# Kernel tuning notes

Hardware: AMD Instinct MI355X
Metric: run time of the kernel (lower is better)

## Reference

```python
import jax, jax.numpy as jnp
import numpy as np

N_HEADS = 8

def _rotate_half(x):
    # interleaved pairs: (x1, x2) -> (-x2, x1), rotary_embedding_torch style
    x = x.reshape(*x.shape[:-1], -1, 2)
    x1, x2 = x[..., 0], x[..., 1]
    return jnp.stack([-x2, x1], axis=-1).reshape(*x.shape[:-2], -1)

def _apply_rotary(freqs, t):
    # freqs: (seq, d), t: (..., seq, d)
    return t * jnp.cos(freqs) + _rotate_half(t) * jnp.sin(freqs)

def _sdpa(q, k, v):
    # q,k,v: (b, g, h, s, d) ; attention over s
    d = q.shape[-1]
    scores = jnp.einsum('bghqd,bghkd->bghqk', q, k) / jnp.sqrt(jnp.asarray(d, q.dtype))
    w = jax.nn.softmax(scores, axis=-1)
    return jnp.einsum('bghqk,bghkd->bghqd', w, v)

def setup_inputs() -> dict:
    key = jax.random.key(0)
    ks = jax.random.split(key, 5)
    B, T, Fd, D = 4, 256, 64, 256
    x = jax.random.normal(ks[0], (B, T, Fd, D), dtype=jnp.float32)
    W_attn = jax.random.normal(ks[1], (D, 5 * D), dtype=jnp.float32) * 0.02
    W_proj = jax.random.normal(ks[2], (D, D), dtype=jnp.float32) * 0.02
    hd = D // N_HEADS
    rotary_t = jax.random.uniform(ks[3], (T, hd), dtype=jnp.float32) * 2 * np.pi
    rotary_f = jax.random.uniform(ks[4], (Fd, hd), dtype=jnp.float32) * 2 * np.pi
    return {"x": x, "W_attn": W_attn, "W_proj": W_proj,
            "rotary_t": rotary_t, "rotary_f": rotary_f}

def reference(x, W_attn, W_proj, rotary_t, rotary_f):
    B, T, Fd, D = x.shape
    h = N_HEADS
    d = D // h
    # fused QKV: (B,T,F,5D) -> (5, B, h, T, F, d)
    qkv = (x @ W_attn).reshape(B, T, Fd, 5, h, d).transpose(3, 0, 4, 1, 2, 5)
    q_t, q_f, k_t, k_f, v = qkv[0], qkv[1], qkv[2], qkv[3], qkv[4]
    # ---- time attention: batch over (b, f), attend over t ----
    # b h t f d -> b f h t d
    q_t = jnp.transpose(q_t, (0, 3, 1, 2, 4))
    k_t = jnp.transpose(k_t, (0, 3, 1, 2, 4))
    v_t = jnp.transpose(v, (0, 3, 1, 2, 4))
    q_t = _apply_rotary(rotary_t, q_t)
    k_t = _apply_rotary(rotary_t, k_t)
    v_t = _sdpa(q_t, k_t, v_t)  # (b, f, h, t, d)
    # ---- frequency attention: batch over (b, t), attend over f ----
    # b h t f d -> b t h f d
    q_f = jnp.transpose(q_f, (0, 2, 1, 3, 4))
    k_f = jnp.transpose(k_f, (0, 2, 1, 3, 4))
    # b f h t d -> b t h f d
    v_f = jnp.transpose(v_t, (0, 3, 2, 1, 4))
    q_f = _apply_rotary(rotary_f, q_f)
    k_f = _apply_rotary(rotary_f, k_f)
    y = _sdpa(q_f, k_f, v_f)  # (b, t, h, f, d)
    # b t h f d -> b t f (h d)
    y = jnp.transpose(y, (0, 1, 3, 2, 4)).reshape(B, T, Fd, D)
    return y @ W_proj
```

## Files before the change

### kernel.cpp

```cpp
#include <hip/hip_runtime.h>

typedef unsigned short u16;
typedef unsigned int u32;
typedef short s16x8 __attribute__((ext_vector_type(8)));
typedef u16 u16x4 __attribute__((ext_vector_type(4)));
typedef float f32x4 __attribute__((ext_vector_type(4)));
typedef u32 u32x2 __attribute__((ext_vector_type(2)));
typedef u32 u32x4 __attribute__((ext_vector_type(4)));

#define MFMA(a,b,c) __builtin_amdgcn_mfma_f32_16x16x32_bf16((a),(b),(c),0,0,0)

static const size_t PL = 16777216;

__device__ __forceinline__ float b2f(u16 b) {
    return __uint_as_float(((unsigned int)b) << 16);
}
__device__ __forceinline__ u16 f2b(float f) {
    unsigned int u = __float_as_uint(f);
    unsigned int r = (u + 0x7FFFu + ((u >> 16) & 1u)) >> 16;
    return (u16)r;
}
__device__ __forceinline__ u32 cvtpk(float lo, float hi) {
    u32 r;
    asm("v_cvt_pk_bf16_f32 %0, %1, %2" : "=v"(r) : "v"(lo), "v"(hi));
    return r;
}
__device__ __forceinline__ float fexp2(float x) {
#if __has_builtin(__builtin_amdgcn_exp2f)
    return __builtin_amdgcn_exp2f(x);
#else
    return exp2f(x);
#endif
}

__device__ __forceinline__ s16x8 rot8(const u16* __restrict__ src,
                                      const float* __restrict__ cp,
                                      const float* __restrict__ sp) {
    s16x8 u = *(const s16x8*)src;
    f32x4 c0 = *(const f32x4*)cp, c1 = *(const f32x4*)(cp + 4);
    f32x4 s0 = *(const f32x4*)sp, s1 = *(const f32x4*)(sp + 4);
    float x[8];
#pragma unroll
    for (int j = 0; j < 8; j++) x[j] = b2f((u16)u[j]);
    float c[8] = {c0[0], c0[1], c0[2], c0[3], c1[0], c1[1], c1[2], c1[3]};
    float s[8] = {s0[0], s0[1], s0[2], s0[3], s1[0], s1[1], s1[2], s1[3]};
    u32x4 r;
#pragma unroll
    for (int p = 0; p < 4; p++) {
        float e = x[2 * p], o = x[2 * p + 1];
        float lo = e * c[2 * p] - o * s[2 * p];
        float hi = fmaf(e, s[2 * p + 1], o * c[2 * p + 1]);
        r[p] = cvtpk(lo, hi);
    }
    return __builtin_bit_cast(s16x8, r);
}

__global__ void prep_x_k(const float* __restrict__ x, u16* __restrict__ xb) {
    size_t i = ((size_t)blockIdx.x * 256 + threadIdx.x) * 8;
    f32x4 a = *(const f32x4*)(x + i);
    f32x4 b = *(const f32x4*)(x + i + 4);
    u32x4 o = { cvtpk(a[0], a[1]), cvtpk(a[2], a[3]), cvtpk(b[0], b[1]), cvtpk(b[2], b[3]) };
    *(u32x4*)(xb + i) = o;
}

__global__ void prep_aux_k(const float* __restrict__ Wa, const float* __restrict__ Wp,
                           const float* __restrict__ rt, const float* __restrict__ rf,
                           u16* __restrict__ wt_a, u16* __restrict__ wt_p,
                           float* __restrict__ ct_t, float* __restrict__ st_t,
                           float* __restrict__ ct_f, float* __restrict__ st_f) {
    int i = blockIdx.x * 256 + threadIdx.x;
    if (i < 81920) {
        int idx = i * 4;
        int k = idx / 1280, n = idx - k * 1280;
        f32x4 v = *(const f32x4*)&Wa[idx];
#pragma unroll
        for (int j = 0; j < 4; j++) wt_a[(n + j) * 256 + k] = f2b(v[j]);
    } else if (i < 98304) {
        int idx = (i - 81920) * 4;
        int k = idx >> 8, n = idx & 255;
        f32x4 v = *(const f32x4*)&Wp[idx];
#pragma unroll
        for (int j = 0; j < 4; j++) wt_p[(n + j) * 256 + k] = f2b(v[j]);
    } else if (i < 100352) {
        int j = (i - 98304) * 4;
        f32x4 v = *(const f32x4*)&rt[j];
        f32x4 c, s;
#pragma unroll
        for (int jj = 0; jj < 4; jj++) { float ss, cc; __sincosf(v[jj], &ss, &cc); c[jj] = cc; s[jj] = ss; }
        *(f32x4*)&ct_t[j] = c; *(f32x4*)&st_t[j] = s;
    } else if (i < 100864) {
        int j = (i - 100352) * 4;
        f32x4 v = *(const f32x4*)&rf[j];
        f32x4 c, s;
#pragma unroll
        for (int jj = 0; jj < 4; jj++) { float ss, cc; __sincosf(v[jj], &ss, &cc); c[jj] = cc; s[jj] = ss; }
        *(f32x4*)&ct_f[j] = c; *(f32x4*)&st_f[j] = s;
    }
}

template<int NT, bool TO_PLANES>
__global__ __launch_bounds__(256, 2) void gemm_k(const u16* __restrict__ A,
                                                 const u16* __restrict__ Bt,
                                                 u16* __restrict__ outp,
                                                 float* __restrict__ outf) {
    __shared__ __align__(16) u16 As[2][128][72];
    __shared__ __align__(16) u16 Bs[2][128][72];
    int bid = blockIdx.x;
    int xcd = bid & 7, slot = bid >> 3;
    int L = xcd * ((512 * NT) / 8) + slot;
    int mt = L / NT, nt = L - mt * NT;
    int m0 = mt * 128, n0 = nt * 128;
    int tid = threadIdx.x, lane = tid & 63, w = tid >> 6;
    int wm = w >> 1, wn = w & 1;
    int g = lane >> 4, lr = lane & 15;
    f32x4 acc[4][4] = {};
    s16x8 apb[4], bpb[4];

    auto loadAB = [&](int k0) {
#pragma unroll
        for (int i = 0; i < 4; i++) {
            int c = tid + i * 256, row = c >> 3, p = (c & 7) * 8;
            apb[i] = *(const s16x8*)&A[(size_t)(m0 + row) * 256 + k0 + p];
            bpb[i] = *(const s16x8*)&Bt[(size_t)(n0 + row) * 256 + k0 + p];
        }
    };
    auto storeAB = [&](int buf) {
#pragma unroll
        for (int i = 0; i < 4; i++) {
            int c = tid + i * 256, row = c >> 3, p = (c & 7) * 8;
            *(s16x8*)&As[buf][row][p] = apb[i];
            *(s16x8*)&Bs[buf][row][p] = bpb[i];
        }
    };

    loadAB(0);
    storeAB(0);
    loadAB(64);
    __syncthreads();

    for (int s = 0; s < 4; s++) {
        int cur = s & 1;
        s16x8 af0[4], bf0[4];
#pragma unroll
        for (int mi = 0; mi < 4; mi++) af0[mi] = *(const s16x8*)&As[cur][wm * 64 + mi * 16 + lr][g * 8];
#pragma unroll
        for (int ni = 0; ni < 4; ni++) bf0[ni] = *(const s16x8*)&Bs[cur][wn * 64 + ni * 16 + lr][g * 8];
        if (s < 3) storeAB(cur ^ 1);
        if (s < 2) loadAB((s + 2) * 64);
#pragma unroll
        for (int ni = 0; ni < 4; ni++)
#pragma unroll
            for (int mi = 0; mi < 4; mi++)
                acc[ni][mi] = MFMA(bf0[ni], af0[mi], acc[ni][mi]);
        s16x8 af1[4], bf1[4];
#pragma unroll
        for (int mi = 0; mi < 4; mi++) af1[mi] = *(const s16x8*)&As[cur][wm * 64 + mi * 16 + lr][32 + g * 8];
#pragma unroll
        for (int ni = 0; ni < 4; ni++) bf1[ni] = *(const s16x8*)&Bs[cur][wn * 64 + ni * 16 + lr][32 + g * 8];
#pragma unroll
        for (int ni = 0; ni < 4; ni++)
#pragma unroll
            for (int mi = 0; mi < 4; mi++)
                acc[ni][mi] = MFMA(bf1[ni], af1[mi], acc[ni][mi]);
        __syncthreads();
    }

#pragma unroll
    for (int ni = 0; ni < 4; ni++) {
#pragma unroll
        for (int mi = 0; mi < 4; mi++) {
            int token = m0 + wm * 64 + mi * 16 + lr;
            int n = n0 + wn * 64 + ni * 16 + g * 4;
            if (TO_PLANES) {
                u32x2 pk = { cvtpk(acc[ni][mi][0], acc[ni][mi][1]),
                             cvtpk(acc[ni][mi][2], acc[ni][mi][3]) };
                int pl = n >> 8, c = n & 255, h = c >> 5, d0 = c & 31;
                int b = token >> 14, t = (token >> 6) & 255, f = token & 63;
                size_t addr = (pl == 1 || pl == 3)
                    ? ((size_t)(((b * 256 + t) * 8 + h) * 64 + f) * 32 + d0)
                    : ((size_t)(((b * 64 + f) * 8 + h) * 256 + t) * 32 + d0);
                *(u32x2*)&outp[(size_t)pl * PL + addr] = pk;
            } else {
                *(f32x4*)&outf[(size_t)token * 256 + n] = acc[ni][mi];
            }
        }
    }
}

__global__ __launch_bounds__(256, 3) void attn_time_k(const u16* __restrict__ qt,
                                                      const u16* __restrict__ kt,
                                                      const u16* __restrict__ vp,
                                                      u16* __restrict__ y1,
                                                      const float* __restrict__ ct,
                                                      const float* __restrict__ st) {
    __shared__ __align__(16) u16 K_l[256][40];
    __shared__ __align__(16) u16 Vt[32][264];
    __shared__ __align__(16) u16 Pst[4][2][16][40];
    int bid = blockIdx.x;
    int xcd = bid & 7, slot = bid >> 3;
    int L = xcd * 512 + slot;
    int qh = L & 1, head = L >> 1;
    int h = head & 7, f = (head >> 3) & 63, b = head >> 9;
    int tid = threadIdx.x, lane = tid & 63, w = tid >> 6;
    int g = lane >> 4, lr = lane & 15;
    const u16* Khead = kt + (size_t)head * 8192;
    const u16* Qhead = qt + (size_t)head * 8192;
    const u16* Vhead = vp + (size_t)head * 8192;

#pragma unroll
    for (int i = 0; i < 4; i++) {
        int c = tid + i * 256;
        int t = c >> 2, p = (c & 3) * 8;
        *(s16x8*)&K_l[t][p] = rot8(Khead + t * 32 + p, ct + t * 32 + p, st + t * 32 + p);
    }
    {
        int ka = (tid & 63) * 4, db = (tid >> 6) * 8;
        const u16* vb = Vhead + (size_t)ka * 32 + db;
        s16x8 r0 = *(const s16x8*)(vb);
        s16x8 r1 = *(const s16x8*)(vb + 32);
        s16x8 r2 = *(const s16x8*)(vb + 64);
        s16x8 r3 = *(const s16x8*)(vb + 96);
#pragma unroll
        for (int dd = 0; dd < 8; dd++) {
            u16x4 pk = { (u16)r0[dd], (u16)r1[dd], (u16)r2[dd], (u16)r3[dd] };
            *(u16x4*)&Vt[db + dd][ka] = pk;
        }
    }
    int qbase = qh * 128 + w * 32;
    s16x8 qf_[2];
#pragma unroll
    for (int qi = 0; qi < 2; qi++) {
        int q = qbase + qi * 16 + lr;
        qf_[qi] = rot8(Qhead + q * 32 + g * 8, ct + q * 32 + g * 8, st + q * 32 + g * 8);
    }
    __syncthreads();

    f32x4 sT[16][2] = {};
#pragma unroll
    for (int ki = 0; ki < 16; ki++) {
        s16x8 kf8 = *(const s16x8*)&K_l[ki * 16 + lr][g * 8];
        sT[ki][0] = MFMA(kf8, qf_[0], sT[ki][0]);
        sT[ki][1] = MFMA(kf8, qf_[1], sT[ki][1]);
    }
    const float sc2 = 0.17677669529663687f * 1.4426950408889634f;
    float rsum[2];
#pragma unroll
    for (int qi = 0; qi < 2; qi++) {
        float m = -1e30f;
#pragma unroll
        for (int ki = 0; ki < 16; ki++)
#pragma unroll
            for (int r = 0; r < 4; r++) m = fmaxf(m, sT[ki][qi][r]);
        m = fmaxf(m, __shfl_xor(m, 16));
        m = fmaxf(m, __shfl_xor(m, 32));
        float msc = m * sc2;
        float ssum = 0.f;
#pragma unroll
        for (int ki = 0; ki < 16; ki++)
#pragma unroll
            for (int r = 0; r < 4; r++) {
                float p = fexp2(sT[ki][qi][r] * sc2 - msc);
                sT[ki][qi][r] = p; ssum += p;
            }
        ssum += __shfl_xor(ssum, 16);
        ssum += __shfl_xor(ssum, 32);
        rsum[qi] = 1.0f / ssum;
    }

    f32x4 o_[2][2] = {};
#pragma unroll
    for (int ks = 0; ks < 8; ks++) {
        s16x8 vf0 = *(const s16x8*)&Vt[lr][ks * 32 + g * 8];
        s16x8 vf1 = *(const s16x8*)&Vt[16 + lr][ks * 32 + g * 8];
#pragma unroll
        for (int qi = 0; qi < 2; qi++) {
            u32x2 w0 = { cvtpk(sT[2 * ks][qi][0], sT[2 * ks][qi][1]),
                         cvtpk(sT[2 * ks][qi][2], sT[2 * ks][qi][3]) };
            u32x2 w1 = { cvtpk(sT[2 * ks + 1][qi][0], sT[2 * ks + 1][qi][1]),
                         cvtpk(sT[2 * ks + 1][qi][2], sT[2 * ks + 1][qi][3]) };
            *(u32x2*)&Pst[w][qi][lr][g * 4] = w0;
            *(u32x2*)&Pst[w][qi][lr][16 + g * 4] = w1;
            s16x8 pf = *(const s16x8*)&Pst[w][qi][lr][g * 8];
            o_[0][qi] = MFMA(vf0, pf, o_[0][qi]);
            o_[1][qi] = MFMA(vf1, pf, o_[1][qi]);
        }
    }
#pragma unroll
    for (int qi = 0; qi < 2; qi++) {
        int q = qbase + qi * 16 + lr;
        float rs = rsum[qi];
        u16* dst = y1 + ((size_t)(((b * 256 + q) * 8 + h) * 64 + f)) * 32;
#pragma unroll
        for (int di = 0; di < 2; di++) {
            u32x2 ob = { cvtpk(o_[di][qi][0] * rs, o_[di][qi][1] * rs),
                         cvtpk(o_[di][qi][2] * rs, o_[di][qi][3] * rs) };
            *(u32x2*)&dst[di * 16 + g * 4] = ob;
        }
    }
}

__global__ __launch_bounds__(256, 2) void attn_freq_k(const u16* __restrict__ qfp,
                                                      const u16* __restrict__ kfp,
                                                      const u16* __restrict__ y1,
                                                      u16* __restrict__ y2,
                                                      const float* __restrict__ ct,
                                                      const float* __restrict__ st) {
    __shared__ __align__(16) u16 K_l[4][64][40];
    __shared__ __align__(16) u16 Vt[4][32][72];
    __shared__ __align__(16) u16 Pst[4][2][16][40];
    int tid = threadIdx.x, lane = tid & 63, w = tid >> 6;
    int g = lane >> 4, lr = lane & 15;
    int head = blockIdx.x * 4 + w;
    int h = head & 7, t = (head >> 3) & 255, b = head >> 11;
    const u16* Khead = kfp + (size_t)head * 2048;
    const u16* Qhead = qfp + (size_t)head * 2048;
    const u16* Vhead = y1 + (size_t)head * 2048;

#pragma unroll
    for (int i = 0; i < 4; i++) {
        int c = i * 64 + lane;
        int row = c >> 2, p = (c & 3) * 8;
        *(s16x8*)&K_l[w][row][p] = rot8(Khead + row * 32 + p, ct + row * 32 + p, st + row * 32 + p);
    }
    {
        int ka = lr * 4, db = g * 8;
        const u16* vb = Vhead + (size_t)ka * 32 + db;
        s16x8 r0 = *(const s16x8*)(vb);
        s16x8 r1 = *(const s16x8*)(vb + 32);
        s16x8 r2 = *(const s16x8*)(vb + 64);
        s16x8 r3 = *(const s16x8*)(vb + 96);
#pragma unroll
        for (int dd = 0; dd < 8; dd++) {
            u16x4 pk = { (u16)r0[dd], (u16)r1[dd], (u16)r2[dd], (u16)r3[dd] };
            *(u16x4*)&Vt[w][db + dd][ka] = pk;
        }
    }
    s16x8 qfr[4];
#pragma unroll
    for (int qi = 0; qi < 4; qi++) {
        int q = qi * 16 + lr;
        qfr[qi] = rot8(Qhead + q * 32 + g * 8, ct + q * 32 + g * 8, st + q * 32 + g * 8);
    }

    f32x4 sT[4][4] = {};
#pragma unroll
    for (int ki = 0; ki < 4; ki++) {
        s16x8 kf8 = *(const s16x8*)&K_l[w][ki * 16 + lr][g * 8];
#pragma unroll
        for (int qi = 0; qi < 4; qi++) sT[ki][qi] = MFMA(kf8, qfr[qi], sT[ki][qi]);
    }
    const float sc2 = 0.17677669529663687f * 1.4426950408889634f;
    float rsum[4];
#pragma unroll
    for (int qi = 0; qi < 4; qi++) {
        float m = -1e30f;
#pragma unroll
        for (int ki = 0; ki < 4; ki++)
#pragma unroll
            for (int r = 0; r < 4; r++) m = fmaxf(m, sT[ki][qi][r]);
        m = fmaxf(m, __shfl_xor(m, 16));
        m = fmaxf(m, __shfl_xor(m, 32));
        float msc = m * sc2;
        float ssum = 0.f;
#pragma unroll
        for (int ki = 0; ki < 4; ki++)
#pragma unroll
            for (int r = 0; r < 4; r++) {
                float p = fexp2(sT[ki][qi][r] * sc2 - msc);
                sT[ki][qi][r] = p; ssum += p;
            }
        ssum += __shfl_xor(ssum, 16);
        ssum += __shfl_xor(ssum, 32);
        rsum[qi] = 1.0f / ssum;
    }

    f32x4 o_[2][4] = {};
#pragma unroll
    for (int ks = 0; ks < 2; ks++) {
        s16x8 vf0 = *(const s16x8*)&Vt[w][lr][ks * 32 + g * 8];
        s16x8 vf1 = *(const s16x8*)&Vt[w][16 + lr][ks * 32 + g * 8];
#pragma unroll
        for (int qi = 0; qi < 4; qi++) {
            u32x2 w0 = { cvtpk(sT[2 * ks][qi][0], sT[2 * ks][qi][1]),
                         cvtpk(sT[2 * ks][qi][2], sT[2 * ks][qi][3]) };
            u32x2 w1 = { cvtpk(sT[2 * ks + 1][qi][0], sT[2 * ks + 1][qi][1]),
                         cvtpk(sT[2 * ks + 1][qi][2], sT[2 * ks + 1][qi][3]) };
            *(u32x2*)&Pst[w][qi & 1][lr][g * 4] = w0;
            *(u32x2*)&Pst[w][qi & 1][lr][16 + g * 4] = w1;
            s16x8 pf = *(const s16x8*)&Pst[w][qi & 1][lr][g * 8];
            o_[0][qi] = MFMA(vf0, pf, o_[0][qi]);
            o_[1][qi] = MFMA(vf1, pf, o_[1][qi]);
        }
    }
#pragma unroll
    for (int qi = 0; qi < 4; qi++) {
        int q = qi * 16 + lr;
        float rs = rsum[qi];
        u16* dst = y2 + ((size_t)((b * 256 + t) * 64 + q)) * 256 + h * 32;
#pragma unroll
        for (int di = 0; di < 2; di++) {
            u32x2 ob = { cvtpk(o_[di][qi][0] * rs, o_[di][qi][1] * rs),
                         cvtpk(o_[di][qi][2] * rs, o_[di][qi][3] * rs) };
            *(u32x2*)&dst[di * 16 + g * 4] = ob;
        }
    }
}

extern "C" void kernel_launch(void* const* d_in, const int* in_sizes, int n_in,
                              void* d_out, int out_size, void* d_ws, size_t ws_size,
                              hipStream_t stream) {
    const float* x  = (const float*)d_in[0];
    const float* Wa = (const float*)d_in[1];
    const float* Wp = (const float*)d_in[2];
    const float* rt = (const float*)d_in[3];
    const float* rf = (const float*)d_in[4];
    float* out = (float*)d_out;

    u16* planes = (u16*)d_ws;
    u16* qt  = planes;
    u16* qfp = planes + PL;
    u16* ktp = planes + 2 * PL;
    u16* kfp = planes + 3 * PL;
    u16* vp  = planes + 4 * PL;
    u16* y1  = planes + 5 * PL;
    u16* xb  = y1;
    u16* y2  = ktp;
    float* ct_t = (float*)(planes + 6 * PL);
    float* st_t = ct_t + 8192;
    float* ct_f = st_t + 8192;
    float* st_f = ct_f + 2048;
    u16* wt_a = (u16*)(st_f + 2048);
    u16* wt_p = wt_a + 327680;

    prep_x_k<<<8192, 256, 0, stream>>>(x, xb);
    prep_aux_k<<<394, 256, 0, stream>>>(Wa, Wp, rt, rf, wt_a, wt_p, ct_t, st_t, ct_f, st_f);
    gemm_k<10, true><<<5120, 256, 0, stream>>>(xb, wt_a, planes, nullptr);
    attn_time_k<<<4096, 256, 0, stream>>>(qt, ktp, vp, y1, ct_t, st_t);
    attn_freq_k<<<2048, 256, 0, stream>>>(qfp, kfp, y1, y2, ct_f, st_f);
    gemm_k<2, false><<<1024, 256, 0, stream>>>(y2, wt_p, nullptr, out);
}
```

Measured before the change: 211.5 us.

## Fuse fp32-to-bf16 conversion of x into QKV GEMM and merge time-attention query halves

The standalone prep_x_k pass is removed, and the QKV GEMM now loads fp32 x directly, converting to bf16 before staging into shared memory. This drops a full write and re-read of the 32 MB-scale bf16 copy of x, at the cost of twice the global load traffic per A tile inside the GEMM and more registers. Separately, attn_time_k now processes both query halves for a head in one block, halving the grid. This avoids rebuilding the rotated K and transposed V tiles twice per head but reduces parallelism and serialises the two halves.

```diff
diff --git a/kernel.cpp b/kernel.cpp
--- a/kernel.cpp
+++ b/kernel.cpp
@@ -53,14 +53,6 @@
         r[p] = cvtpk(lo, hi);
     }
     return __builtin_bit_cast(s16x8, r);
-}
-
-__global__ void prep_x_k(const float* __restrict__ x, u16* __restrict__ xb) {
-    size_t i = ((size_t)blockIdx.x * 256 + threadIdx.x) * 8;
-    f32x4 a = *(const f32x4*)(x + i);
-    f32x4 b = *(const f32x4*)(x + i + 4);
-    u32x4 o = { cvtpk(a[0], a[1]), cvtpk(a[2], a[3]), cvtpk(b[0], b[1]), cvtpk(b[2], b[3]) };
-    *(u32x4*)(xb + i) = o;
 }
 
 __global__ void prep_aux_k(const float* __restrict__ Wa, const float* __restrict__ Wp,
@@ -98,13 +90,15 @@
     }
 }
 
-template<int NT, bool TO_PLANES>
-__global__ __launch_bounds__(256, 2) void gemm_k(const u16* __restrict__ A,
+template<int NT, bool AF32, bool TO_PLANES>
+__global__ __launch_bounds__(256, 2) void gemm_k(const void* __restrict__ Ap,
                                                  const u16* __restrict__ Bt,
                                                  u16* __restrict__ outp,
                                                  float* __restrict__ outf) {
     __shared__ __align__(16) u16 As[2][128][72];
     __shared__ __align__(16) u16 Bs[2][128][72];
+    const float* Af = (const float*)Ap;
+    const u16* Ab = (const u16*)Ap;
     int bid = blockIdx.x;
     int xcd = bid & 7, slot = bid >> 3;
     int L = xcd * ((512 * NT) / 8) + slot;
@@ -114,21 +108,46 @@
     int wm = w >> 1, wn = w & 1;
     int g = lane >> 4, lr = lane & 15;
     f32x4 acc[4][4] = {};
-    s16x8 apb[4], bpb[4];
+    f32x4 apf[8]; s16x8 apb[4]; s16x8 bpb[4];
 
     auto loadAB = [&](int k0) {
+        if (AF32) {
+#pragma unroll
+            for (int i = 0; i < 8; i++) {
+                int c = tid + i * 256, row = c >> 4, cp = (c & 15) * 4;
+                apf[i] = *(const f32x4*)&Af[(size_t)(m0 + row) * 256 + k0 + cp];
+            }
+        } else {
+#pragma unroll
+            for (int i = 0; i < 4; i++) {
+                int c = tid + i * 256, row = c >> 3, p = (c & 7) * 8;
+                apb[i] = *(const s16x8*)&Ab[(size_t)(m0 + row) * 256 + k0 + p];
+            }
+        }
 #pragma unroll
         for (int i = 0; i < 4; i++) {
             int c = tid + i * 256, row = c >> 3, p = (c & 7) * 8;
-            apb[i] = *(const s16x8*)&A[(size_t)(m0 + row) * 256 + k0 + p];
             bpb[i] = *(const s16x8*)&Bt[(size_t)(n0 + row) * 256 + k0 + p];
         }
     };
     auto storeAB = [&](int buf) {
+        if (AF32) {
+#pragma unroll
+            for (int i = 0; i < 8; i++) {
+                int c = tid + i * 256, row = c >> 4, cp = (c & 15) * 4;
+                u32x2 pk = { cvtpk(apf[i][0], apf[i][1]), cvtpk(apf[i][2], apf[i][3]) };
+                *(u32x2*)&As[buf][row][cp] = pk;
+            }
+        } else {
+#pragma unroll
+            for (int i = 0; i < 4; i++) {
+                int c = tid + i * 256, row = c >> 3, p = (c & 7) * 8;
+                *(s16x8*)&As[buf][row][p] = apb[i];
+            }
+        }
 #pragma unroll
         for (int i = 0; i < 4; i++) {
             int c = tid + i * 256, row = c >> 3, p = (c & 7) * 8;
-            *(s16x8*)&As[buf][row][p] = apb[i];
             *(s16x8*)&Bs[buf][row][p] = bpb[i];
         }
     };
@@ -198,8 +217,7 @@
     __shared__ __align__(16) u16 Pst[4][2][16][40];
     int bid = blockIdx.x;
     int xcd = bid & 7, slot = bid >> 3;
-    int L = xcd * 512 + slot;
-    int qh = L & 1, head = L >> 1;
+    int head = xcd * 256 + slot;
     int h = head & 7, f = (head >> 3) & 63, b = head >> 9;
     int tid = threadIdx.x, lane = tid & 63, w = tid >> 6;
     int g = lane >> 4, lr = lane & 15;
@@ -226,75 +244,78 @@
             *(u16x4*)&Vt[db + dd][ka] = pk;
         }
     }
-    int qbase = qh * 128 + w * 32;
-    s16x8 qf_[2];
-#pragma unroll
-    for (int qi = 0; qi < 2; qi++) {
-        int q = qbase + qi * 16 + lr;
-        qf_[qi] = rot8(Qhead + q * 32 + g * 8, ct + q * 32 + g * 8, st + q * 32 + g * 8);
-    }
     __syncthreads();
 
-    f32x4 sT[16][2] = {};
-#pragma unroll
-    for (int ki = 0; ki < 16; ki++) {
-        s16x8 kf8 = *(const s16x8*)&K_l[ki * 16 + lr][g * 8];
-        sT[ki][0] = MFMA(kf8, qf_[0], sT[ki][0]);
-        sT[ki][1] = MFMA(kf8, qf_[1], sT[ki][1]);
-    }
     const float sc2 = 0.17677669529663687f * 1.4426950408889634f;
-    float rsum[2];
-#pragma unroll
-    for (int qi = 0; qi < 2; qi++) {
-        float m = -1e30f;
-#pragma unroll
-        for (int ki = 0; ki < 16; ki++)
-#pragma unroll
-            for (int r = 0; r < 4; r++) m = fmaxf(m, sT[ki][qi][r]);
-        m = fmaxf(m, __shfl_xor(m, 16));
-        m = fmaxf(m, __shfl_xor(m, 32));
-        float msc = m * sc2;
-        float ssum = 0.f;
-#pragma unroll
-        for (int ki = 0; ki < 16; ki++)
-#pragma unroll
-            for (int r = 0; r < 4; r++) {
-                float p = fexp2(sT[ki][qi][r] * sc2 - msc);
-                sT[ki][qi][r] = p; ssum += p;
-            }
-        ssum += __shfl_xor(ssum, 16);
-        ssum += __shfl_xor(ssum, 32);
-        rsum[qi] = 1.0f / ssum;
-    }
-
-    f32x4 o_[2][2] = {};
-#pragma unroll
-    for (int ks = 0; ks < 8; ks++) {
-        s16x8 vf0 = *(const s16x8*)&Vt[lr][ks * 32 + g * 8];
-        s16x8 vf1 = *(const s16x8*)&Vt[16 + lr][ks * 32 + g * 8];
+    for (int qh = 0; qh < 2; qh++) {
+        int qbase = qh * 128 + w * 32;
+        s16x8 qf_[2];
 #pragma unroll
         for (int qi = 0; qi < 2; qi++) {
-            u32x2 w0 = { cvtpk(sT[2 * ks][qi][0], sT[2 * ks][qi][1]),
-                         cvtpk(sT[2 * ks][qi][2], sT[2 * ks][qi][3]) };
-            u32x2 w1 = { cvtpk(sT[2 * ks + 1][qi][0], sT[2 * ks + 1][qi][1]),
-                         cvtpk(sT[2 * ks + 1][qi][2], sT[2 * ks + 1][qi][3]) };
-            *(u32x2*)&Pst[w][qi][lr][g * 4] = w0;
-            *(u32x2*)&Pst[w][qi][lr][16 + g * 4] = w1;
-            s16x8 pf = *(const s16x8*)&Pst[w][qi][lr][g * 8];
-            o_[0][qi] = MFMA(vf0, pf, o_[0][qi]);
-            o_[1][qi] = MFMA(vf1, pf, o_[1][qi]);
-        }
-    }
-#pragma unroll
-    for (int qi = 0; qi < 2; qi++) {
-        int q = qbase + qi * 16 + lr;
-        float rs = rsum[qi];
-        u16* dst = y1 + ((size_t)(((b * 256 + q) * 8 + h) * 64 + f)) * 32;
-#pragma unroll
-        for (int di = 0; di < 2; di++) {
-            u32x2 ob = { cvtpk(o_[di][qi][0] * rs, o_[di][qi][1] * rs),
-                         cvtpk(o_[di][qi][2] * rs, o_[di][qi][3] * rs) };
-            *(u32x2*)&dst[di * 16 + g * 4] = ob;
+            int q = qbase + qi * 16 + lr;
+            qf_[qi] = rot8(Qhead + q * 32 + g * 8, ct + q * 32 + g * 8, st + q * 32 + g * 8);
+        }
+
+        f32x4 sT[16][2] = {};
+#pragma unroll
+        for (int ki = 0; ki < 16; ki++) {
+            s16x8 kf8 = *(const s16x8*)&K_l[ki * 16 + lr][g * 8];
+            sT[ki][0] = MFMA(kf8, qf_[0], sT[ki][0]);
+            sT[ki][1] = MFMA(kf8, qf_[1], sT[ki][1]);
+        }
+        float rsum[2];
+#pragma unroll
+        for (int qi = 0; qi < 2; qi++) {
+            float m = -1e30f;
+#pragma unroll
+            for (int ki = 0; ki < 16; ki++)
+#pragma unroll
+                for (int r = 0; r < 4; r++) m = fmaxf(m, sT[ki][qi][r]);
+            m = fmaxf(m, __shfl_xor(m, 16));
+            m = fmaxf(m, __shfl_xor(m, 32));
+            float msc = m * sc2;
+            float ssum = 0.f;
+#pragma unroll
+            for (int ki = 0; ki < 16; ki++)
+#pragma unroll
+                for (int r = 0; r < 4; r++) {
+                    float p = fexp2(sT[ki][qi][r] * sc2 - msc);
+                    sT[ki][qi][r] = p; ssum += p;
+                }
+            ssum += __shfl_xor(ssum, 16);
+            ssum += __shfl_xor(ssum, 32);
+            rsum[qi] = 1.0f / ssum;
+        }
+
+        f32x4 o_[2][2] = {};
+#pragma unroll
+        for (int ks = 0; ks < 8; ks++) {
+            s16x8 vf0 = *(const s16x8*)&Vt[lr][ks * 32 + g * 8];
+            s16x8 vf1 = *(const s16x8*)&Vt[16 + lr][ks * 32 + g * 8];
+#pragma unroll
+            for (int qi = 0; qi < 2; qi++) {
+                u32x2 w0 = { cvtpk(sT[2 * ks][qi][0], sT[2 * ks][qi][1]),
+                             cvtpk(sT[2 * ks][qi][2], sT[2 * ks][qi][3]) };
+                u32x2 w1 = { cvtpk(sT[2 * ks + 1][qi][0], sT[2 * ks + 1][qi][1]),
+                             cvtpk(sT[2 * ks + 1][qi][2], sT[2 * ks + 1][qi][3]) };
+                *(u32x2*)&Pst[w][qi][lr][g * 4] = w0;
+                *(u32x2*)&Pst[w][qi][lr][16 + g * 4] = w1;
+                s16x8 pf = *(const s16x8*)&Pst[w][qi][lr][g * 8];
+                o_[0][qi] = MFMA(vf0, pf, o_[0][qi]);
+                o_[1][qi] = MFMA(vf1, pf, o_[1][qi]);
+            }
+        }
+#pragma unroll
+        for (int qi = 0; qi < 2; qi++) {
+            int q = qbase + qi * 16 + lr;
+            float rs = rsum[qi];
+            u16* dst = y1 + ((size_t)(((b * 256 + q) * 8 + h) * 64 + f)) * 32;
+#pragma unroll
+            for (int di = 0; di < 2; di++) {
+                u32x2 ob = { cvtpk(o_[di][qi][0] * rs, o_[di][qi][1] * rs),
+                             cvtpk(o_[di][qi][2] * rs, o_[di][qi][3] * rs) };
+                *(u32x2*)&dst[di * 16 + g * 4] = ob;
+            }
         }
     }
 }
@@ -423,7 +444,6 @@
     u16* kfp = planes + 3 * PL;
     u16* vp  = planes + 4 * PL;
     u16* y1  = planes + 5 * PL;
-    u16* xb  = y1;
     u16* y2  = ktp;
     float* ct_t = (float*)(planes + 6 * PL);
     float* st_t = ct_t + 8192;
@@ -432,10 +452,9 @@
     u16* wt_a = (u16*)(st_f + 2048);
     u16* wt_p = wt_a + 327680;
 
-    prep_x_k<<<8192, 256, 0, stream>>>(x, xb);
     prep_aux_k<<<394, 256, 0, stream>>>(Wa, Wp, rt, rf, wt_a, wt_p, ct_t, st_t, ct_f, st_f);
-    gemm_k<10, true><<<5120, 256, 0, stream>>>(xb, wt_a, planes, nullptr);
-    attn_time_k<<<4096, 256, 0, stream>>>(qt, ktp, vp, y1, ct_t, st_t);
+    gemm_k<10, true, true><<<5120, 256, 0, stream>>>(x, wt_a, planes, nullptr);
+    attn_time_k<<<2048, 256, 0, stream>>>(qt, ktp, vp, y1, ct_t, st_t);
     attn_freq_k<<<2048, 256, 0, stream>>>(qfp, kfp, y1, y2, ct_f, st_f);
-    gemm_k<2, false><<<1024, 256, 0, stream>>>(y2, wt_p, nullptr, out);
-}
+    gemm_k<2, false, false><<<1024, 256, 0, stream>>>(y2, wt_p, nullptr, out);
+}
```

Result: slower. 259.9 us (+22.9%).
